# Optimization experiments

Measured on AMD Instinct MI355X. Metric: run time of the kernel, lower is better.

The kernel has to match this reference:

```python
import jax, jax.numpy as jnp
import numpy as np


def setup_inputs() -> dict:
    key = jax.random.key(0)
    k1, k2 = jax.random.split(key)
    N, C = 2097152, 40
    input = jax.random.normal(k1, (N, C), dtype=jnp.float32)
    raw = jax.random.uniform(k2, (N, C), dtype=jnp.float32)
    # target rows are probability distributions (as in soft-label CE usage)
    target = raw / jnp.sum(raw, axis=-1, keepdims=True)
    return {"input": input, "target": target}


def reference(input, target):
    # Soft-label cross entropy: loss_i = -sum_c target[i,c] * log_softmax(input)[i,c]
    # (equivalent to the per-class looped F.cross_entropy in the original,
    #  but computes log_softmax once). reduction='mean', weight=None.
    logp = jax.nn.log_softmax(input, axis=-1)  # [N, C]
    per_point = -jnp.sum(target * logp, axis=-1)  # [N]
    return jnp.mean(per_point)
```

## Files before the change

### kernel.cpp

```cpp
#include <hip/hip_runtime.h>
#include <math.h>


#define THREADS 256
#define BLOCKS  2048
#define UNROLL  4
#define C       40
#define F4ROW   10

typedef float vf4 __attribute__((ext_vector_type(4)));

__global__ __launch_bounds__(THREADS) void ce_coal(
    const float* __restrict__ input,
    const float* __restrict__ target,
    float* __restrict__ partials, int N)
{
    const int lane  = threadIdx.x & 63;
    const int wib   = threadIdx.x >> 6;
    const int gw    = blockIdx.x * (THREADS / 64) + wib;
    const int nw    = gridDim.x * (THREADS / 64);
    const int seg   = lane / 10;
    const int cpos  = lane - seg * 10;
    const bool laneOn = (lane < 60);
    const int G = (N + 5) / 6;

    const vf4* xg = reinterpret_cast<const vf4*>(input);
    const vf4* tg = reinterpret_cast<const vf4*>(target);

    float acc = 0.f;
    for (long long g0 = (long long)gw * UNROLL; g0 < G;
         g0 += (long long)nw * UNROLL)
    {
        vf4 xv[UNROLL], tv[UNROLL];
        bool act[UNROLL];

        #pragma unroll
        for (int u = 0; u < UNROLL; ++u) {
            const long long g = g0 + u;
            const int row = (int)(g * 6) + seg;
            const bool a = laneOn && (g < (long long)G) && (row < N);
            act[u] = a;
            const size_t idx = (size_t)g * 60 + lane;
            if (a) {
                xv[u] = __builtin_nontemporal_load(xg + idx);
                tv[u] = __builtin_nontemporal_load(tg + idx);
            } else {
                xv[u] = (vf4)0.f;
                tv[u] = (vf4)0.f;
            }
        }

        #pragma unroll
        for (int u = 0; u < UNROLL; ++u) {
            float se = 0.f, dot = 0.f, ts = 0.f;
            if (act[u]) {
                const vf4 x = xv[u], t = tv[u];
                se  = __expf(x.x) + __expf(x.y) + __expf(x.z) + __expf(x.w);
                dot = t.x * x.x + t.y * x.y + t.z * x.z + t.w * x.w;
                ts  = t.x + t.y + t.z + t.w;
            }
            #define SEGRED(OFF) {                                   \
                const float a1 = __shfl_down(se,  OFF, 64);         \
                const float a2 = __shfl_down(dot, OFF, 64);         \
                const float a3 = __shfl_down(ts,  OFF, 64);         \
                if (cpos + OFF < 10) { se += a1; dot += a2; ts += a3; } }
            SEGRED(1) SEGRED(2) SEGRED(4) SEGRED(8)
            #undef SEGRED

            if (cpos == 0 && act[u])
                acc += ts * __logf(se) - dot;
        }
    }

    #pragma unroll
    for (int off = 32; off > 0; off >>= 1) acc += __shfl_down(acc, off, 64);
    __shared__ float sdata[THREADS / 64];
    if (lane == 0) sdata[wib] = acc;
    __syncthreads();
    if (threadIdx.x == 0) {
        float s = 0.f;
        #pragma unroll
        for (int w = 0; w < THREADS / 64; ++w) s += sdata[w];
        partials[blockIdx.x] = s;
    }
}

__global__ __launch_bounds__(256) void ce_final(
    const float* __restrict__ partials, float* __restrict__ out,
    int nPartials, float invN)
{
    float acc = 0.f;
    for (int i = threadIdx.x; i < nPartials; i += blockDim.x) acc += partials[i];
    #pragma unroll
    for (int off = 32; off > 0; off >>= 1) acc += __shfl_down(acc, off, 64);
    __shared__ float sdata[4];
    const int lane = threadIdx.x & 63, wid = threadIdx.x >> 6;
    if (lane == 0) sdata[wid] = acc;
    __syncthreads();
    if (threadIdx.x == 0)
        out[0] = (sdata[0] + sdata[1] + sdata[2] + sdata[3]) * invN;
}

extern "C" void kernel_launch(void* const* d_in, const int* in_sizes, int n_in,
                              void* d_out, int out_size, void* d_ws, size_t ws_size,
                              hipStream_t stream)
{
    const float* input  = (const float*)d_in[0];
    const float* target = (const float*)d_in[1];
    float* out = (float*)d_out;
    float* partials = (float*)d_ws;

    const int N = in_sizes[0] / C;

    ce_coal<<<BLOCKS, THREADS, 0, stream>>>(input, target, partials, N);
    ce_final<<<1, 256, 0, stream>>>(partials, out, BLOCKS, 1.0f / (float)N);
}
```

Measured before the change: 114.3 us.

## Fuse final reduction via last-block atomic counter and use contiguous per-wave chunks

Replaces the separate final-reduction kernel with a last-block-done pattern: each block bumps an atomic counter and the last one sums all partials and writes the mean. Also changes the work split from a grid-stride interleave to a contiguous range of row groups per wave. The goal is to drop one kernel launch and improve streaming locality per wave. In exchange it adds a memset launch for the counter, plus fences and an atomic per block.

Result: slower. 220.8 us (+93.2%).

```diff
diff --git a/kernel.cpp b/kernel.cpp
--- a/kernel.cpp
+++ b/kernel.cpp
@@ -6,14 +6,16 @@
 #define BLOCKS  2048
 #define UNROLL  4
 #define C       40
-#define F4ROW   10
 
 typedef float vf4 __attribute__((ext_vector_type(4)));
 
-__global__ __launch_bounds__(THREADS) void ce_coal(
+__global__ __launch_bounds__(THREADS) void ce_fused(
     const float* __restrict__ input,
     const float* __restrict__ target,
-    float* __restrict__ partials, int N)
+    float* __restrict__ partials,
+    unsigned int* __restrict__ counter,
+    float* __restrict__ out,
+    int N, float invN)
 {
     const int lane  = threadIdx.x & 63;
     const int wib   = threadIdx.x >> 6;
@@ -24,21 +26,23 @@
     const bool laneOn = (lane < 60);
     const int G = (N + 5) / 6;
 
+    const int q = G / nw, r = G % nw;
+    const int cnt = q + (gw < r ? 1 : 0);
+    const long long base = (long long)gw * q + (gw < r ? gw : r);
+
     const vf4* xg = reinterpret_cast<const vf4*>(input);
     const vf4* tg = reinterpret_cast<const vf4*>(target);
 
     float acc = 0.f;
-    for (long long g0 = (long long)gw * UNROLL; g0 < G;
-         g0 += (long long)nw * UNROLL)
-    {
+    for (int i = 0; i < cnt; i += UNROLL) {
         vf4 xv[UNROLL], tv[UNROLL];
         bool act[UNROLL];
 
         #pragma unroll
         for (int u = 0; u < UNROLL; ++u) {
-            const long long g = g0 + u;
+            const long long g = base + i + u;
             const int row = (int)(g * 6) + seg;
-            const bool a = laneOn && (g < (long long)G) && (row < N);
+            const bool a = laneOn && (i + u < cnt) && (row < N);
             act[u] = a;
             const size_t idx = (size_t)g * 60 + lane;
             if (a) {
@@ -83,22 +87,32 @@
         for (int w = 0; w < THREADS / 64; ++w) s += sdata[w];
         partials[blockIdx.x] = s;
     }
-}
 
-__global__ __launch_bounds__(256) void ce_final(
-    const float* __restrict__ partials, float* __restrict__ out,
-    int nPartials, float invN)
-{
-    float acc = 0.f;
-    for (int i = threadIdx.x; i < nPartials; i += blockDim.x) acc += partials[i];
-    #pragma unroll
-    for (int off = 32; off > 0; off >>= 1) acc += __shfl_down(acc, off, 64);
-    __shared__ float sdata[4];
-    const int lane = threadIdx.x & 63, wid = threadIdx.x >> 6;
-    if (lane == 0) sdata[wid] = acc;
+    __shared__ bool amLast;
+    if (threadIdx.x == 0) {
+        __threadfence();
+        const unsigned int prev = atomicAdd(counter, 1u);
+        amLast = (prev == (unsigned int)gridDim.x - 1u);
+    }
     __syncthreads();
-    if (threadIdx.x == 0)
-        out[0] = (sdata[0] + sdata[1] + sdata[2] + sdata[3]) * invN;
+    if (amLast) {
+        __threadfence();
+        float s = 0.f;
+        for (int i = threadIdx.x; i < BLOCKS; i += THREADS)
+            s += __hip_atomic_load(&partials[i], __ATOMIC_RELAXED,
+                                   __HIP_MEMORY_SCOPE_AGENT);
+        #pragma unroll
+        for (int off = 32; off > 0; off >>= 1) s += __shfl_down(s, off, 64);
+        __shared__ float fdata[THREADS / 64];
+        if (lane == 0) fdata[wib] = s;
+        __syncthreads();
+        if (threadIdx.x == 0) {
+            float tot = 0.f;
+            #pragma unroll
+            for (int w = 0; w < THREADS / 64; ++w) tot += fdata[w];
+            out[0] = tot * invN;
+        }
+    }
 }
 
 extern "C" void kernel_launch(void* const* d_in, const int* in_sizes, int n_in,
@@ -108,10 +122,13 @@
     const float* input  = (const float*)d_in[0];
     const float* target = (const float*)d_in[1];
     float* out = (float*)d_out;
-    float* partials = (float*)d_ws;
+
+    unsigned int* counter = (unsigned int*)d_ws;
+    float* partials = (float*)((char*)d_ws + 256);
 
     const int N = in_sizes[0] / C;
 
-    ce_coal<<<BLOCKS, THREADS, 0, stream>>>(input, target, partials, N);
-    ce_final<<<1, 256, 0, stream>>>(partials, out, BLOCKS, 1.0f / (float)N);
+    hipMemsetAsync(counter, 0, sizeof(unsigned int), stream);
+    ce_fused<<<BLOCKS, THREADS, 0, stream>>>(input, target, partials, counter,
+                                             out, N, 1.0f / (float)N);
 }
```
